# Optimization experiments

Hardware: AMD Instinct MI355X
Metric: run time of the kernel (lower is better)

Reference implementation:

```python
import jax, jax.numpy as jnp
import numpy as np

DIM = 1024
DEPTH = 7
PAR = 8
N_NODES = 2 ** (DEPTH + 1) - 1  # 255
WIDTH = PAR * N_NODES  # 2040


def setup_inputs() -> dict:
    key = jax.random.key(0)
    k1, k2, k3, k4 = jax.random.split(key, 4)
    init_k = float(np.sqrt(1.0 / DIM))
    init_k2 = float(np.sqrt(1.0 / ((DEPTH + 1) * PAR)))
    oldx = jax.random.normal(k1, (4, 2048, DIM), dtype=jnp.float32)
    W_in = jax.random.uniform(k2, (WIDTH, DIM), jnp.float32, -init_k, init_k)
    b_in = jax.random.uniform(k3, (WIDTH,), jnp.float32, -init_k, init_k)
    W_out = jax.random.uniform(k4, (DIM, WIDTH), jnp.float32, -init_k2, init_k2)
    return {"oldx": oldx, "W_in": W_in, "b_in": b_in, "W_out": W_out}


def reference(oldx, W_in, b_in, W_out):
    x = oldx.reshape(-1, DIM)                      # [B, dim]
    B = x.shape[0]
    logits = x @ W_in.T + b_in                     # [B, width] dense GEMM over ALL nodes
    decisions = (logits > 0).astype(jnp.int32).reshape(B, PAR, N_NODES)
    acts = jax.nn.silu(logits).reshape(B, PAR, N_NODES)

    # Tree traversal: mark root, then descend DEPTH levels by each node's sign bit.
    current = jnp.zeros((B, PAR), dtype=jnp.int32)
    dmap = jax.nn.one_hot(current, N_NODES, dtype=acts.dtype)  # root node marked
    for d in range(DEPTH):
        cur_platform = 2 ** d - 1
        next_platform = 2 ** (d + 1) - 1
        moves = jnp.take_along_axis(decisions, current[..., None], axis=2)[..., 0]
        current = (current - cur_platform) * 2 + moves + next_platform
        dmap = dmap + jax.nn.one_hot(current, N_NODES, dtype=acts.dtype)

    masked = acts * jax.lax.stop_gradient(dmap)    # only depth+1 nodes per tree survive
    out = masked.reshape(B, WIDTH) @ W_out.T       # [B, dim]
    return out.reshape(oldx.shape)
```

## Files before the change

kernel.cpp:

```cpp
#include <hip/hip_runtime.h>
#include <math.h>

#define DIM 1024
#define DEPTH 7
#define PAR 8
#define N_NODES 255
#define WIDTH 2040
#define MARGIN 0.01f

#define REPLANE(p) ((((p) & 1) << 3) | ((((p) >> 1) & 1) << 4) | ((((p) >> 2) & 1) << 5))

typedef _Float16 half2v __attribute__((ext_vector_type(2)));

__device__ __forceinline__ half2v as_h2(unsigned int u) {
    union { unsigned int u; half2v h; } c; c.u = u; return c.h;
}
__device__ __forceinline__ unsigned int pack_h2(float a, float b) {
    union { half2v h; unsigned int u; } c;
    c.h = (half2v){(_Float16)a, (_Float16)b};
    return c.u;
}

__device__ __forceinline__ float dot2h(unsigned int a, unsigned int b, float c) {
#if __has_builtin(__builtin_amdgcn_fdot2)
    return __builtin_amdgcn_fdot2(as_h2(a), as_h2(b), c, false);
#else
    half2v ha = as_h2(a), hb = as_h2(b);
    c = fmaf((float)ha.x, (float)hb.x, c);
    return fmaf((float)ha.y, (float)hb.y, c);
#endif
}

__device__ __forceinline__ float foldK(float a, float b, int K) {
    const bool hi = (threadIdx.x & (unsigned)K) != 0;
    const float keep = hi ? b : a;
    const float send = hi ? a : b;
    return keep + __shfl_xor(send, K, 64);
}

#define TRANS_BLOCKS 512

__global__ __launch_bounds__(256) void prep_kernel(
    const float* __restrict__ W_out,
    const float* __restrict__ W_in,
    unsigned short* __restrict__ WoT,
    unsigned int* __restrict__ Wh)
{
    __shared__ float tile[64][65];
    if (blockIdx.x < TRANS_BLOCKS) {
        const int w0 = (int)(blockIdx.x & 31) * 64;
        const int d0 = (int)(blockIdx.x >> 5) * 64;
        const int tid = (int)threadIdx.x;
        const int sub = tid & 15;
        const int grp = tid >> 4;

        #pragma unroll
        for (int pass = 0; pass < 4; ++pass) {
            const int dl = pass * 16 + grp;
            const int wl = sub * 4;
            const int w = w0 + wl;
            const int d = d0 + dl;
            float4 v = make_float4(0.f, 0.f, 0.f, 0.f);
            if (w + 3 < WIDTH) {
                v = *(const float4*)(W_out + (size_t)d * WIDTH + w);
            } else {
                float t0 = (w + 0 < WIDTH) ? W_out[(size_t)d * WIDTH + w + 0] : 0.f;
                float t1 = (w + 1 < WIDTH) ? W_out[(size_t)d * WIDTH + w + 1] : 0.f;
                float t2 = (w + 2 < WIDTH) ? W_out[(size_t)d * WIDTH + w + 2] : 0.f;
                float t3 = (w + 3 < WIDTH) ? W_out[(size_t)d * WIDTH + w + 3] : 0.f;
                v = make_float4(t0, t1, t2, t3);
            }
            tile[dl][wl + 0] = v.x; tile[dl][wl + 1] = v.y;
            tile[dl][wl + 2] = v.z; tile[dl][wl + 3] = v.w;
        }
        __syncthreads();
        #pragma unroll
        for (int pass = 0; pass < 4; ++pass) {
            const int wl = pass * 16 + grp;
            const int dl = sub * 4;
            const int w = w0 + wl;
            if (w < WIDTH) {
                uint2 pk;
                pk.x = pack_h2(tile[dl + 0][wl], tile[dl + 1][wl]);
                pk.y = pack_h2(tile[dl + 2][wl], tile[dl + 3][wl]);
                *(uint2*)(WoT + (size_t)w * DIM + d0 + dl) = pk;
            }
        }
    } else {
        const int n4 = WIDTH * DIM / 4;
        const int nthr = ((int)gridDim.x - TRANS_BLOCKS) * 256;
        for (int i = ((int)blockIdx.x - TRANS_BLOCKS) * 256 + (int)threadIdx.x;
             i < n4; i += nthr) {
            float4 v = ((const float4*)W_in)[i];
            uint2 pk;
            pk.x = pack_h2(v.x, v.y);
            pk.y = pack_h2(v.z, v.w);
            ((uint2*)Wh)[i] = pk;
        }
    }
}

__global__ __launch_bounds__(256) void fff_stage1_kernel(
    const float* __restrict__ x,
    const float* __restrict__ W_in,
    const float* __restrict__ b_in,
    const unsigned int* __restrict__ Wh,
    float* __restrict__ acts,
    unsigned short* __restrict__ gidx_out,
    int B)
{
    const int wv = (int)((blockIdx.x * blockDim.x + threadIdx.x) >> 6);
    const int lane = (int)(threadIdx.x & 63);
    const int rowA = wv * 2;
    const int rowB = wv * 2 + 1;
    if (rowA >= B) return;
    const bool hasB = (rowB < B);

    const float* xrA = x + (size_t)rowA * DIM;
    const float* xrB = x + (size_t)(hasB ? rowB : rowA) * DIM;

    unsigned int xpA[8], xpB[8];
    {
        float4 a0 = *(const float4*)(xrA + lane * 8 + 0);
        float4 a1 = *(const float4*)(xrA + lane * 8 + 4);
        float4 a2 = *(const float4*)(xrA + 512 + lane * 8 + 0);
        float4 a3 = *(const float4*)(xrA + 512 + lane * 8 + 4);
        xpA[0] = pack_h2(a0.x, a0.y); xpA[1] = pack_h2(a0.z, a0.w);
        xpA[2] = pack_h2(a1.x, a1.y); xpA[3] = pack_h2(a1.z, a1.w);
        xpA[4] = pack_h2(a2.x, a2.y); xpA[5] = pack_h2(a2.z, a2.w);
        xpA[6] = pack_h2(a3.x, a3.y); xpA[7] = pack_h2(a3.z, a3.w);
        float4 b0 = *(const float4*)(xrB + lane * 8 + 0);
        float4 b1 = *(const float4*)(xrB + lane * 8 + 4);
        float4 b2 = *(const float4*)(xrB + 512 + lane * 8 + 0);
        float4 b3 = *(const float4*)(xrB + 512 + lane * 8 + 4);
        xpB[0] = pack_h2(b0.x, b0.y); xpB[1] = pack_h2(b0.z, b0.w);
        xpB[2] = pack_h2(b1.x, b1.y); xpB[3] = pack_h2(b1.z, b1.w);
        xpB[4] = pack_h2(b2.x, b2.y); xpB[5] = pack_h2(b2.z, b2.w);
        xpB[6] = pack_h2(b3.x, b3.y); xpB[7] = pack_h2(b3.z, b3.w);
    }

    unsigned long long nodesA = 0ULL, nodesB = 0ULL;
    const int myp = ((lane >> 3) & 1) | (((lane >> 4) & 1) << 1) | (((lane >> 5) & 1) << 2);

    #pragma unroll 1
    for (int d = 0; d <= DEPTH; ++d) {
        int gA[PAR], gB[PAR];
        #pragma unroll
        for (int p = 0; p < PAR; ++p) {
            gA[p] = p * N_NODES + (int)((nodesA >> (8 * p)) & 0xffULL);
            gB[p] = p * N_NODES + (int)((nodesB >> (8 * p)) & 0xffULL);
        }

        const int gaA = (lane & 8) ? gA[1] : gA[0];
        const int gbA = (lane & 8) ? gA[3] : gA[2];
        const int gcA = (lane & 8) ? gA[5] : gA[4];
        const int gdA = (lane & 8) ? gA[7] : gA[6];
        const int geA = (lane & 16) ? gbA : gaA;
        const int gfA = (lane & 16) ? gdA : gcA;
        const int gmineA = (lane & 32) ? gfA : geA;
        const float biasA = b_in[gmineA];
        const int gaB = (lane & 8) ? gB[1] : gB[0];
        const int gbB = (lane & 8) ? gB[3] : gB[2];
        const int gcB = (lane & 8) ? gB[5] : gB[4];
        const int gdB = (lane & 8) ? gB[7] : gB[6];
        const int geB = (lane & 16) ? gbB : gaB;
        const int gfB = (lane & 16) ? gdB : gcB;
        const int gmineB = (lane & 32) ? gfB : geB;
        const float biasB = b_in[gmineB];

        float pA[PAR], pB[PAR];
        uint4 a0, a1, b0, b1;
        {
            const unsigned int* wrA = Wh + (size_t)gA[0] * (DIM / 2);
            a0 = *(const uint4*)(wrA + lane * 4);
            a1 = *(const uint4*)(wrA + 256 + lane * 4);
            const unsigned int* wrB = Wh + (size_t)gB[0] * (DIM / 2);
            b0 = *(const uint4*)(wrB + lane * 4);
            b1 = *(const uint4*)(wrB + 256 + lane * 4);
        }
        #pragma unroll
        for (int p = 0; p < PAR; ++p) {
            uint4 na0 = a0, na1 = a1, nb0 = b0, nb1 = b1;
            if (p < PAR - 1) {
                const unsigned int* wrA = Wh + (size_t)gA[p + 1] * (DIM / 2);
                na0 = *(const uint4*)(wrA + lane * 4);
                na1 = *(const uint4*)(wrA + 256 + lane * 4);
                const unsigned int* wrB = Wh + (size_t)gB[p + 1] * (DIM / 2);
                nb0 = *(const uint4*)(wrB + lane * 4);
                nb1 = *(const uint4*)(wrB + 256 + lane * 4);
            }
            float s = 0.f;
            s = dot2h(xpA[0], a0.x, s);
            s = dot2h(xpA[1], a0.y, s);
            s = dot2h(xpA[2], a0.z, s);
            s = dot2h(xpA[3], a0.w, s);
            s = dot2h(xpA[4], a1.x, s);
            s = dot2h(xpA[5], a1.y, s);
            s = dot2h(xpA[6], a1.z, s);
            s = dot2h(xpA[7], a1.w, s);
            pA[p] = s;
            float t = 0.f;
            t = dot2h(xpB[0], b0.x, t);
            t = dot2h(xpB[1], b0.y, t);
            t = dot2h(xpB[2], b0.z, t);
            t = dot2h(xpB[3], b0.w, t);
            t = dot2h(xpB[4], b1.x, t);
            t = dot2h(xpB[5], b1.y, t);
            t = dot2h(xpB[6], b1.z, t);
            t = dot2h(xpB[7], b1.w, t);
            pB[p] = t;
            a0 = na0; a1 = na1; b0 = nb0; b1 = nb1;
        }

        const float cA01 = foldK(pA[0], pA[1], 8);
        const float cB01 = foldK(pB[0], pB[1], 8);
        const float cA23 = foldK(pA[2], pA[3], 8);
        const float cB23 = foldK(pB[2], pB[3], 8);
        const float cA45 = foldK(pA[4], pA[5], 8);
        const float cB45 = foldK(pB[4], pB[5], 8);
        const float cA67 = foldK(pA[6], pA[7], 8);
        const float cB67 = foldK(pB[6], pB[7], 8);
        const float dA0 = foldK(cA01, cA23, 16);
        const float dB0 = foldK(cB01, cB23, 16);
        const float dA1 = foldK(cA45, cA67, 16);
        const float dB1 = foldK(cB45, cB67, 16);
        float eA = foldK(dA0, dA1, 32);
        float eB = foldK(dB0, dB1, 32);
        eA += __shfl_xor(eA, 1, 64);  eB += __shfl_xor(eB, 1, 64);
        eA += __shfl_xor(eA, 2, 64);  eB += __shfl_xor(eB, 2, 64);
        eA += __shfl_xor(eA, 4, 64);  eB += __shfl_xor(eB, 4, 64);
        float myA = eA + biasA;
        float myB = eB + biasB;

        if (d < DEPTH) {
            const unsigned long long balA = __ballot(fabsf(myA) < MARGIN);
            unsigned rmA = 0;
            #pragma unroll
            for (int p = 0; p < PAR; ++p)
                rmA |= ((unsigned)((balA >> REPLANE(p)) & 1ULL)) << p;
            while (rmA) {
                const int p = __builtin_ctz(rmA); rmA &= (rmA - 1u);
                const int gi = p * N_NODES + (int)((nodesA >> (8 * p)) & 0xffULL);
                const float* wr = W_in + (size_t)gi * DIM;
                float s = 0.f;
                #pragma unroll
                for (int q = 0; q < 4; ++q) {
                    const int off = (q & 1) * 4 + (q >> 1) * 512 + lane * 8;
                    const float4 fx = *(const float4*)(xrA + off);
                    const float4 fw = *(const float4*)(wr + off);
                    s = fmaf(fx.x, fw.x, s); s = fmaf(fx.y, fw.y, s);
                    s = fmaf(fx.z, fw.z, s); s = fmaf(fx.w, fw.w, s);
                }
                #pragma unroll
                for (int off = 32; off >= 1; off >>= 1)
                    s += __shfl_xor(s, off, 64);
                const float lf = s + b_in[gi];
                myA = (myp == p) ? lf : myA;
            }
            const unsigned long long balB = __ballot(fabsf(myB) < MARGIN);
            unsigned rmB = 0;
            #pragma unroll
            for (int p = 0; p < PAR; ++p)
                rmB |= ((unsigned)((balB >> REPLANE(p)) & 1ULL)) << p;
            while (rmB) {
                const int p = __builtin_ctz(rmB); rmB &= (rmB - 1u);
                const int gi = p * N_NODES + (int)((nodesB >> (8 * p)) & 0xffULL);
                const float* wr = W_in + (size_t)gi * DIM;
                float s = 0.f;
                #pragma unroll
                for (int q = 0; q < 4; ++q) {
                    const int off = (q & 1) * 4 + (q >> 1) * 512 + lane * 8;
                    const float4 fx = *(const float4*)(xrB + off);
                    const float4 fw = *(const float4*)(wr + off);
                    s = fmaf(fx.x, fw.x, s); s = fmaf(fx.y, fw.y, s);
                    s = fmaf(fx.z, fw.z, s); s = fmaf(fx.w, fw.w, s);
                }
                #pragma unroll
                for (int off = 32; off >= 1; off >>= 1)
                    s += __shfl_xor(s, off, 64);
                const float lf = s + b_in[gi];
                myB = (myp == p) ? lf : myB;
            }
        }

        const float actA = myA / (1.0f + __expf(-myA));
        const float actB = myB / (1.0f + __expf(-myB));
        const unsigned long long posA = __ballot(myA > 0.0f);
        const unsigned long long posB = __ballot(myB > 0.0f);

        if ((lane & 7) == 0) {
            const int slotA = (rowA << 6) + (d << 3) + myp;
            acts[slotA] = actA;
            gidx_out[slotA] = (unsigned short)gmineA;
            if (hasB) {
                const int slotB = (rowB << 6) + (d << 3) + myp;
                acts[slotB] = actB;
                gidx_out[slotB] = (unsigned short)gmineB;
            }
        }

        if (d < DEPTH) {
            #pragma unroll
            for (int p = 0; p < PAR; ++p) {
                const int npA = (int)((nodesA >> (8 * p)) & 0xffULL);
                const unsigned long long nnA = (unsigned long long)
                    (2 * npA + 1 + (int)((posA >> REPLANE(p)) & 1ULL));
                nodesA = (nodesA & ~(0xffULL << (8 * p))) | (nnA << (8 * p));
                const int npB = (int)((nodesB >> (8 * p)) & 0xffULL);
                const unsigned long long nnB = (unsigned long long)
                    (2 * npB + 1 + (int)((posB >> REPLANE(p)) & 1ULL));
                nodesB = (nodesB & ~(0xffULL << (8 * p))) | (nnB << (8 * p));
            }
        }
    }
}

__global__ __launch_bounds__(256) void fff_stage2_kernel(
    const float* __restrict__ acts,
    const unsigned short* __restrict__ gidx16,
    const unsigned short* __restrict__ WoT,
    float* __restrict__ out,
    int B)
{
    const int wave = (int)((blockIdx.x * blockDim.x + threadIdx.x) >> 6);
    const int lane = (int)(threadIdx.x & 63);
    if (wave >= B) return;

    const int base = wave << 6;
    const float a_l = acts[base + lane];
    const int   g_l = (int)gidx16[base + lane];

    float acc[16];
    #pragma unroll
    for (int i = 0; i < 16; ++i) acc[i] = 0.f;

    #pragma unroll 4
    for (int e = 0; e < 64; ++e) {
        const float a_ = __shfl(a_l, e, 64);
        const int   g  = __shfl(g_l, e, 64);
        const unsigned short* wo = WoT + (size_t)g * DIM;
        const uint4 u0 = *(const uint4*)(wo + lane * 8);
        const uint4 u1 = *(const uint4*)(wo + 512 + lane * 8);
        half2v h_;
        h_ = as_h2(u0.x); acc[0]  = fmaf((float)h_.x, a_, acc[0]);  acc[1]  = fmaf((float)h_.y, a_, acc[1]);
        h_ = as_h2(u0.y); acc[2]  = fmaf((float)h_.x, a_, acc[2]);  acc[3]  = fmaf((float)h_.y, a_, acc[3]);
        h_ = as_h2(u0.z); acc[4]  = fmaf((float)h_.x, a_, acc[4]);  acc[5]  = fmaf((float)h_.y, a_, acc[5]);
        h_ = as_h2(u0.w); acc[6]  = fmaf((float)h_.x, a_, acc[6]);  acc[7]  = fmaf((float)h_.y, a_, acc[7]);
        h_ = as_h2(u1.x); acc[8]  = fmaf((float)h_.x, a_, acc[8]);  acc[9]  = fmaf((float)h_.y, a_, acc[9]);
        h_ = as_h2(u1.y); acc[10] = fmaf((float)h_.x, a_, acc[10]); acc[11] = fmaf((float)h_.y, a_, acc[11]);
        h_ = as_h2(u1.z); acc[12] = fmaf((float)h_.x, a_, acc[12]); acc[13] = fmaf((float)h_.y, a_, acc[13]);
        h_ = as_h2(u1.w); acc[14] = fmaf((float)h_.x, a_, acc[14]); acc[15] = fmaf((float)h_.y, a_, acc[15]);
    }

    float* orow = out + (size_t)wave * DIM;
    *(float4*)(orow + lane * 8 + 0)       = make_float4(acc[0],  acc[1],  acc[2],  acc[3]);
    *(float4*)(orow + lane * 8 + 4)       = make_float4(acc[4],  acc[5],  acc[6],  acc[7]);
    *(float4*)(orow + 512 + lane * 8 + 0) = make_float4(acc[8],  acc[9],  acc[10], acc[11]);
    *(float4*)(orow + 512 + lane * 8 + 4) = make_float4(acc[12], acc[13], acc[14], acc[15]);
}

__global__ __launch_bounds__(256) void fff_f16_kernel(
    const float* __restrict__ x,
    const float* __restrict__ W_in,
    const float* __restrict__ b_in,
    const unsigned int* __restrict__ Wh,
    const unsigned short* __restrict__ WoT,
    float* __restrict__ out,
    int B)
{
    const int wave = (int)((blockIdx.x * blockDim.x + threadIdx.x) >> 6);
    const int lane = (int)(threadIdx.x & 63);
    if (wave >= B) return;

    const float* xr = x + (size_t)wave * DIM;
    unsigned int xp[8];
    {
        float4 a0 = *(const float4*)(xr + lane * 8 + 0);
        float4 a1 = *(const float4*)(xr + lane * 8 + 4);
        float4 a2 = *(const float4*)(xr + 512 + lane * 8 + 0);
        float4 a3 = *(const float4*)(xr + 512 + lane * 8 + 4);
        xp[0] = pack_h2(a0.x, a0.y);
        xp[1] = pack_h2(a0.z, a0.w);
        xp[2] = pack_h2(a1.x, a1.y);
        xp[3] = pack_h2(a1.z, a1.w);
        xp[4] = pack_h2(a2.x, a2.y);
        xp[5] = pack_h2(a2.z, a2.w);
        xp[6] = pack_h2(a3.x, a3.y);
        xp[7] = pack_h2(a3.z, a3.w);
    }

    float acc[16];
    #pragma unroll
    for (int i = 0; i < 16; ++i) acc[i] = 0.f;

    unsigned long long nodes = 0ULL;
    const int myp = ((lane >> 3) & 1) | (((lane >> 4) & 1) << 1) | (((lane >> 5) & 1) << 2);

    #pragma unroll 1
    for (int d = 0; d <= DEPTH; ++d) {
        int gidx[PAR];
        #pragma unroll
        for (int p = 0; p < PAR; ++p) {
            const int np = (int)((nodes >> (8 * p)) & 0xffULL);
            gidx[p] = p * N_NODES + np;
        }

        const int ga = (lane & 8) ? gidx[1] : gidx[0];
        const int gb = (lane & 8) ? gidx[3] : gidx[2];
        const int gc = (lane & 8) ? gidx[5] : gidx[4];
        const int gd = (lane & 8) ? gidx[7] : gidx[6];
        const int ge = (lane & 16) ? gb : ga;
        const int gf = (lane & 16) ? gd : gc;
        const int gmine = (lane & 32) ? gf : ge;
        const float bias = b_in[gmine];

        float partial[PAR];
        #pragma unroll
        for (int p = 0; p < PAR; ++p) {
            const unsigned int* wr = Wh + (size_t)gidx[p] * (DIM / 2);
            const uint4 u0 = *(const uint4*)(wr + lane * 4);
            const uint4 u1 = *(const uint4*)(wr + 256 + lane * 4);
            float s = 0.f;
            s = dot2h(xp[0], u0.x, s);
            s = dot2h(xp[1], u0.y, s);
            s = dot2h(xp[2], u0.z, s);
            s = dot2h(xp[3], u0.w, s);
            s = dot2h(xp[4], u1.x, s);
            s = dot2h(xp[5], u1.y, s);
            s = dot2h(xp[6], u1.z, s);
            s = dot2h(xp[7], u1.w, s);
            partial[p] = s;
        }

        const float c01 = foldK(partial[0], partial[1], 8);
        const float c23 = foldK(partial[2], partial[3], 8);
        const float c45 = foldK(partial[4], partial[5], 8);
        const float c67 = foldK(partial[6], partial[7], 8);
        const float d0f = foldK(c01, c23, 16);
        const float d1f = foldK(c45, c67, 16);
        float e = foldK(d0f, d1f, 32);
        e += __shfl_xor(e, 1, 64);
        e += __shfl_xor(e, 2, 64);
        e += __shfl_xor(e, 4, 64);
        float my = e + bias;

        if (d < DEPTH) {
            const unsigned long long bal = __ballot(fabsf(my) < MARGIN);
            unsigned rm = 0;
            #pragma unroll
            for (int p = 0; p < PAR; ++p)
                rm |= ((unsigned)((bal >> REPLANE(p)) & 1ULL)) << p;
            if (rm) {
                while (rm) {
                    const int p = __builtin_ctz(rm); rm &= (rm - 1u);
                    const int np = (int)((nodes >> (8 * p)) & 0xffULL);
                    const int gi = p * N_NODES + np;
                    const float* wr = W_in + (size_t)gi * DIM;
                    float s = 0.f;
                    #pragma unroll
                    for (int q = 0; q < 4; ++q) {
                        const int off = (q & 1) * 4 + (q >> 1) * 512 + lane * 8;
                        const float4 fx = *(const float4*)(xr + off);
                        const float4 fw = *(const float4*)(wr + off);
                        s = fmaf(fx.x, fw.x, s); s = fmaf(fx.y, fw.y, s);
                        s = fmaf(fx.z, fw.z, s); s = fmaf(fx.w, fw.w, s);
                    }
                    #pragma unroll
                    for (int off = 32; off >= 1; off >>= 1)
                        s += __shfl_xor(s, off, 64);
                    const float lf = s + b_in[gi];
                    my = (myp == p) ? lf : my;
                }
            }
        }

        const float act_mine = my / (1.0f + __expf(-my));
        const unsigned long long pos = __ballot(my > 0.0f);

        float act[PAR];
        #pragma unroll
        for (int p = 0; p < PAR; ++p)
            act[p] = __shfl(act_mine, REPLANE(p), 64);

        #pragma unroll
        for (int p = 0; p < PAR; ++p) {
            const unsigned short* wo = WoT + (size_t)gidx[p] * DIM;
            const uint4 u0 = *(const uint4*)(wo + lane * 8);
            const uint4 u1 = *(const uint4*)(wo + 512 + lane * 8);
            const float a_ = act[p];
            half2v h_;
            h_ = as_h2(u0.x); acc[0]  = fmaf((float)h_.x, a_, acc[0]);  acc[1]  = fmaf((float)h_.y, a_, acc[1]);
            h_ = as_h2(u0.y); acc[2]  = fmaf((float)h_.x, a_, acc[2]);  acc[3]  = fmaf((float)h_.y, a_, acc[3]);
            h_ = as_h2(u0.z); acc[4]  = fmaf((float)h_.x, a_, acc[4]);  acc[5]  = fmaf((float)h_.y, a_, acc[5]);
            h_ = as_h2(u0.w); acc[6]  = fmaf((float)h_.x, a_, acc[6]);  acc[7]  = fmaf((float)h_.y, a_, acc[7]);
            h_ = as_h2(u1.x); acc[8]  = fmaf((float)h_.x, a_, acc[8]);  acc[9]  = fmaf((float)h_.y, a_, acc[9]);
            h_ = as_h2(u1.y); acc[10] = fmaf((float)h_.x, a_, acc[10]); acc[11] = fmaf((float)h_.y, a_, acc[11]);
            h_ = as_h2(u1.z); acc[12] = fmaf((float)h_.x, a_, acc[12]); acc[13] = fmaf((float)h_.y, a_, acc[13]);
            h_ = as_h2(u1.w); acc[14] = fmaf((float)h_.x, a_, acc[14]); acc[15] = fmaf((float)h_.y, a_, acc[15]);

            if (d < DEPTH) {
                const int np = (int)((nodes >> (8 * p)) & 0xffULL);
                const unsigned long long nn = (unsigned long long)
                    (2 * np + 1 + (int)((pos >> REPLANE(p)) & 1ULL));
                nodes = (nodes & ~(0xffULL << (8 * p))) | (nn << (8 * p));
            }
        }
    }

    float* orow = out + (size_t)wave * DIM;
    *(float4*)(orow + lane * 8 + 0)       = make_float4(acc[0],  acc[1],  acc[2],  acc[3]);
    *(float4*)(orow + lane * 8 + 4)       = make_float4(acc[4],  acc[5],  acc[6],  acc[7]);
    *(float4*)(orow + 512 + lane * 8 + 0) = make_float4(acc[8],  acc[9],  acc[10], acc[11]);
    *(float4*)(orow + 512 + lane * 8 + 4) = make_float4(acc[12], acc[13], acc[14], acc[15]);
}

__global__ __launch_bounds__(256) void fff_fallback_kernel(
    const float* __restrict__ x, const float* __restrict__ W_in,
    const float* __restrict__ b_in, const float* __restrict__ W_out,
    float* __restrict__ out, int B)
{
    const int wave = (int)((blockIdx.x * blockDim.x + threadIdx.x) >> 6);
    const int lane = (int)(threadIdx.x & 63);
    if (wave >= B) return;

    const float* xr = x + (size_t)wave * DIM;
    float4 x4[4];
    x4[0] = *(const float4*)(xr + lane * 8 + 0);
    x4[1] = *(const float4*)(xr + lane * 8 + 4);
    x4[2] = *(const float4*)(xr + 512 + lane * 8 + 0);
    x4[3] = *(const float4*)(xr + 512 + lane * 8 + 4);

    float acc[16];
    #pragma unroll
    for (int i = 0; i < 16; ++i) acc[i] = 0.f;
    int node[PAR];
    #pragma unroll
    for (int p = 0; p < PAR; ++p) node[p] = 0;

    for (int d = 0; d <= DEPTH; ++d) {
        #pragma unroll
        for (int p = 0; p < PAR; ++p) {
            const int gidx = p * N_NODES + node[p];
            const float* wr = W_in + (size_t)gidx * DIM;
            const float4 wa = *(const float4*)(wr + lane * 8 + 0);
            const float4 wb = *(const float4*)(wr + lane * 8 + 4);
            const float4 wc = *(const float4*)(wr + 512 + lane * 8 + 0);
            const float4 wd = *(const float4*)(wr + 512 + lane * 8 + 4);
            float s = 0.f;
            s = fmaf(x4[0].x, wa.x, s); s = fmaf(x4[0].y, wa.y, s);
            s = fmaf(x4[0].z, wa.z, s); s = fmaf(x4[0].w, wa.w, s);
            s = fmaf(x4[1].x, wb.x, s); s = fmaf(x4[1].y, wb.y, s);
            s = fmaf(x4[1].z, wb.z, s); s = fmaf(x4[1].w, wb.w, s);
            s = fmaf(x4[2].x, wc.x, s); s = fmaf(x4[2].y, wc.y, s);
            s = fmaf(x4[2].z, wc.z, s); s = fmaf(x4[2].w, wc.w, s);
            s = fmaf(x4[3].x, wd.x, s); s = fmaf(x4[3].y, wd.y, s);
            s = fmaf(x4[3].z, wd.z, s); s = fmaf(x4[3].w, wd.w, s);
            #pragma unroll
            for (int off = 32; off >= 1; off >>= 1)
                s += __shfl_xor(s, off, 64);
            const float logit = s + b_in[gidx];
            const float act = logit / (1.0f + __expf(-logit));
            #pragma unroll
            for (int k = 0; k < 2; ++k) {
                #pragma unroll
                for (int j = 0; j < 8; ++j) {
                    const int e = k * 512 + lane * 8 + j;
                    acc[k * 8 + j] = fmaf(act, W_out[(size_t)e * WIDTH + gidx], acc[k * 8 + j]);
                }
            }
            node[p] = 2 * node[p] + 1 + ((logit > 0.0f) ? 1 : 0);
        }
    }

    float* orow = out + (size_t)wave * DIM;
    *(float4*)(orow + lane * 8 + 0)       = make_float4(acc[0],  acc[1],  acc[2],  acc[3]);
    *(float4*)(orow + lane * 8 + 4)       = make_float4(acc[4],  acc[5],  acc[6],  acc[7]);
    *(float4*)(orow + 512 + lane * 8 + 0) = make_float4(acc[8],  acc[9],  acc[10], acc[11]);
    *(float4*)(orow + 512 + lane * 8 + 4) = make_float4(acc[12], acc[13], acc[14], acc[15]);
}

extern "C" void kernel_launch(void* const* d_in, const int* in_sizes, int n_in,
                              void* d_out, int out_size, void* d_ws, size_t ws_size,
                              hipStream_t stream) {
    const float* oldx  = (const float*)d_in[0];
    const float* W_in  = (const float*)d_in[1];
    const float* b_in  = (const float*)d_in[2];
    const float* W_out = (const float*)d_in[3];
    float* out = (float*)d_out;

    const int B = in_sizes[0] / DIM;

    const size_t half   = (size_t)WIDTH * DIM * sizeof(unsigned short);
    const size_t actsz  = (size_t)B * 64 * sizeof(float);
    const size_t idxsz  = (size_t)B * 64 * sizeof(unsigned short);
    const bool use_split = (d_ws != nullptr) && (ws_size >= 2 * half + actsz + idxsz);
    const bool use_lp    = (d_ws != nullptr) && (ws_size >= 2 * half);

    const int blocks = (B + 3) / 4;

    if (use_split) {
        unsigned short* WoT  = (unsigned short*)d_ws;
        unsigned int*   Wh   = (unsigned int*)((char*)d_ws + half);
        float*          acts = (float*)((char*)d_ws + 2 * half);
        unsigned short* gidx = (unsigned short*)((char*)d_ws + 2 * half + actsz);
        prep_kernel<<<TRANS_BLOCKS + 1024, 256, 0, stream>>>(W_out, W_in, WoT, Wh);
        const int wavesS1 = (B + 1) / 2;
        const int blocksS1 = (wavesS1 + 3) / 4;
        fff_stage1_kernel<<<blocksS1, 256, 0, stream>>>(oldx, W_in, b_in, Wh, acts, gidx, B);
        fff_stage2_kernel<<<blocks, 256, 0, stream>>>(acts, gidx, WoT, out, B);
    } else if (use_lp) {
        unsigned short* WoT = (unsigned short*)d_ws;
        unsigned int*   Wh  = (unsigned int*)((char*)d_ws + half);
        prep_kernel<<<TRANS_BLOCKS + 1024, 256, 0, stream>>>(W_out, W_in, WoT, Wh);
        fff_f16_kernel<<<blocks, 256, 0, stream>>>(oldx, W_in, b_in, Wh, WoT, out, B);
    } else {
        fff_fallback_kernel<<<blocks, 256, 0, stream>>>(oldx, W_in, b_in, W_out, out, B);
    }
}
```

Measured before the change: 179.1 us.

## Fuse tree-routing stage and output projection into one two-row-per-wave kernel

Merges the two-stage split (a stage-1 kernel writing activations and node indices to workspace, then a stage-2 gather GEMV) into a single kernel. Each wave handles two rows, computes the routing logits, and immediately accumulates the selected W_out columns into register accumulators. This removes the intermediate workspace round-trip and one kernel launch. In exchange it doubles the accumulator registers (32 floats plus the packed x values), which may lower occupancy. It also removes the one-row-per-wave f16 kernel path.

```diff
diff --git a/kernel.cpp b/kernel.cpp
--- a/kernel.cpp
+++ b/kernel.cpp
@@ -100,13 +100,13 @@
     }
 }
 
-__global__ __launch_bounds__(256) void fff_stage1_kernel(
+__global__ __launch_bounds__(256) void fff_fused2_kernel(
     const float* __restrict__ x,
     const float* __restrict__ W_in,
     const float* __restrict__ b_in,
     const unsigned int* __restrict__ Wh,
-    float* __restrict__ acts,
-    unsigned short* __restrict__ gidx_out,
+    const unsigned short* __restrict__ WoT,
+    float* __restrict__ out,
     int B)
 {
     const int wv = (int)((blockIdx.x * blockDim.x + threadIdx.x) >> 6);
@@ -138,6 +138,10 @@
         xpB[4] = pack_h2(b2.x, b2.y); xpB[5] = pack_h2(b2.z, b2.w);
         xpB[6] = pack_h2(b3.x, b3.y); xpB[7] = pack_h2(b3.z, b3.w);
     }
+
+    float accA[16], accB[16];
+    #pragma unroll
+    for (int i = 0; i < 16; ++i) { accA[i] = 0.f; accB[i] = 0.f; }
 
     unsigned long long nodesA = 0ULL, nodesB = 0ULL;
     const int myp = ((lane >> 3) & 1) | (((lane >> 4) & 1) << 1) | (((lane >> 5) & 1) << 2);
@@ -288,15 +292,35 @@
         const unsigned long long posA = __ballot(myA > 0.0f);
         const unsigned long long posB = __ballot(myB > 0.0f);
 
-        if ((lane & 7) == 0) {
-            const int slotA = (rowA << 6) + (d << 3) + myp;
-            acts[slotA] = actA;
-            gidx_out[slotA] = (unsigned short)gmineA;
-            if (hasB) {
-                const int slotB = (rowB << 6) + (d << 3) + myp;
-                acts[slotB] = actB;
-                gidx_out[slotB] = (unsigned short)gmineB;
-            }
+        #pragma unroll
+        for (int p = 0; p < PAR; ++p) {
+            const int gAp = p * N_NODES + (int)((nodesA >> (8 * p)) & 0xffULL);
+            const float aA = __shfl(actA, REPLANE(p), 64);
+            const unsigned short* woA = WoT + (size_t)gAp * DIM;
+            const uint4 u0 = *(const uint4*)(woA + lane * 8);
+            const uint4 u1 = *(const uint4*)(woA + 512 + lane * 8);
+            const int gBp = p * N_NODES + (int)((nodesB >> (8 * p)) & 0xffULL);
+            const float aB = __shfl(actB, REPLANE(p), 64);
+            const unsigned short* woB = WoT + (size_t)gBp * DIM;
+            const uint4 v0 = *(const uint4*)(woB + lane * 8);
+            const uint4 v1 = *(const uint4*)(woB + 512 + lane * 8);
+            half2v h_;
+            h_ = as_h2(u0.x); accA[0]  = fmaf((float)h_.x, aA, accA[0]);  accA[1]  = fmaf((float)h_.y, aA, accA[1]);
+            h_ = as_h2(u0.y); accA[2]  = fmaf((float)h_.x, aA, accA[2]);  accA[3]  = fmaf((float)h_.y, aA, accA[3]);
+            h_ = as_h2(u0.z); accA[4]  = fmaf((float)h_.x, aA, accA[4]);  accA[5]  = fmaf((float)h_.y, aA, accA[5]);
+            h_ = as_h2(u0.w); accA[6]  = fmaf((float)h_.x, aA, accA[6]);  accA[7]  = fmaf((float)h_.y, aA, accA[7]);
+            h_ = as_h2(u1.x); accA[8]  = fmaf((float)h_.x, aA, accA[8]);  accA[9]  = fmaf((float)h_.y, aA, accA[9]);
+            h_ = as_h2(u1.y); accA[10] = fmaf((float)h_.x, aA, accA[10]); accA[11] = fmaf((float)h_.y, aA, accA[11]);
+            h_ = as_h2(u1.z); accA[12] = fmaf((float)h_.x, aA, accA[12]); accA[13] = fmaf((float)h_.y, aA, accA[13]);
+            h_ = as_h2(u1.w); accA[14] = fmaf((float)h_.x, aA, accA[14]); accA[15] = fmaf((float)h_.y, aA, accA[15]);
+            h_ = as_h2(v0.x); accB[0]  = fmaf((float)h_.x, aB, accB[0]);  accB[1]  = fmaf((float)h_.y, aB, accB[1]);
+            h_ = as_h2(v0.y); accB[2]  = fmaf((float)h_.x, aB, accB[2]);  accB[3]  = fmaf((float)h_.y, aB, accB[3]);
+            h_ = as_h2(v0.z); accB[4]  = fmaf((float)h_.x, aB, accB[4]);  accB[5]  = fmaf((float)h_.y, aB, accB[5]);
+            h_ = as_h2(v0.w); accB[6]  = fmaf((float)h_.x, aB, accB[6]);  accB[7]  = fmaf((float)h_.y, aB, accB[7]);
+            h_ = as_h2(v1.x); accB[8]  = fmaf((float)h_.x, aB, accB[8]);  accB[9]  = fmaf((float)h_.y, aB, accB[9]);
+            h_ = as_h2(v1.y); accB[10] = fmaf((float)h_.x, aB, accB[10]); accB[11] = fmaf((float)h_.y, aB, accB[11]);
+            h_ = as_h2(v1.z); accB[12] = fmaf((float)h_.x, aB, accB[12]); accB[13] = fmaf((float)h_.y, aB, accB[13]);
+            h_ = as_h2(v1.w); accB[14] = fmaf((float)h_.x, aB, accB[14]); accB[15] = fmaf((float)h_.y, aB, accB[15]);
         }
 
         if (d < DEPTH) {
@@ -313,205 +337,19 @@
             }
         }
     }
-}
-
-__global__ __launch_bounds__(256) void fff_stage2_kernel(
-    const float* __restrict__ acts,
-    const unsigned short* __restrict__ gidx16,
-    const unsigned short* __restrict__ WoT,
-    float* __restrict__ out,
-    int B)
-{
-    const int wave = (int)((blockIdx.x * blockDim.x + threadIdx.x) >> 6);
-    const int lane = (int)(threadIdx.x & 63);
-    if (wave >= B) return;
-
-    const int base = wave << 6;
-    const float a_l = acts[base + lane];
-    const int   g_l = (int)gidx16[base + lane];
-
-    float acc[16];
-    #pragma unroll
-    for (int i = 0; i < 16; ++i) acc[i] = 0.f;
-
-    #pragma unroll 4
-    for (int e = 0; e < 64; ++e) {
-        const float a_ = __shfl(a_l, e, 64);
-        const int   g  = __shfl(g_l, e, 64);
-        const unsigned short* wo = WoT + (size_t)g * DIM;
-        const uint4 u0 = *(const uint4*)(wo + lane * 8);
-        const uint4 u1 = *(const uint4*)(wo + 512 + lane * 8);
-        half2v h_;
-        h_ = as_h2(u0.x); acc[0]  = fmaf((float)h_.x, a_, acc[0]);  acc[1]  = fmaf((float)h_.y, a_, acc[1]);
-        h_ = as_h2(u0.y); acc[2]  = fmaf((float)h_.x, a_, acc[2]);  acc[3]  = fmaf((float)h_.y, a_, acc[3]);
-        h_ = as_h2(u0.z); acc[4]  = fmaf((float)h_.x, a_, acc[4]);  acc[5]  = fmaf((float)h_.y, a_, acc[5]);
-        h_ = as_h2(u0.w); acc[6]  = fmaf((float)h_.x, a_, acc[6]);  acc[7]  = fmaf((float)h_.y, a_, acc[7]);
-        h_ = as_h2(u1.x); acc[8]  = fmaf((float)h_.x, a_, acc[8]);  acc[9]  = fmaf((float)h_.y, a_, acc[9]);
-        h_ = as_h2(u1.y); acc[10] = fmaf((float)h_.x, a_, acc[10]); acc[11] = fmaf((float)h_.y, a_, acc[11]);
-        h_ = as_h2(u1.z); acc[12] = fmaf((float)h_.x, a_, acc[12]); acc[13] = fmaf((float)h_.y, a_, acc[13]);
-        h_ = as_h2(u1.w); acc[14] = fmaf((float)h_.x, a_, acc[14]); acc[15] = fmaf((float)h_.y, a_, acc[15]);
-    }
-
-    float* orow = out + (size_t)wave * DIM;
-    *(float4*)(orow + lane * 8 + 0)       = make_float4(acc[0],  acc[1],  acc[2],  acc[3]);
-    *(float4*)(orow + lane * 8 + 4)       = make_float4(acc[4],  acc[5],  acc[6],  acc[7]);
-    *(float4*)(orow + 512 + lane * 8 + 0) = make_float4(acc[8],  acc[9],  acc[10], acc[11]);
-    *(float4*)(orow + 512 + lane * 8 + 4) = make_float4(acc[12], acc[13], acc[14], acc[15]);
-}
-
-__global__ __launch_bounds__(256) void fff_f16_kernel(
-    const float* __restrict__ x,
-    const float* __restrict__ W_in,
-    const float* __restrict__ b_in,
-    const unsigned int* __restrict__ Wh,
-    const unsigned short* __restrict__ WoT,
-    float* __restrict__ out,
-    int B)
-{
-    const int wave = (int)((blockIdx.x * blockDim.x + threadIdx.x) >> 6);
-    const int lane = (int)(threadIdx.x & 63);
-    if (wave >= B) return;
-
-    const float* xr = x + (size_t)wave * DIM;
-    unsigned int xp[8];
-    {
-        float4 a0 = *(const float4*)(xr + lane * 8 + 0);
-        float4 a1 = *(const float4*)(xr + lane * 8 + 4);
-        float4 a2 = *(const float4*)(xr + 512 + lane * 8 + 0);
-        float4 a3 = *(const float4*)(xr + 512 + lane * 8 + 4);
-        xp[0] = pack_h2(a0.x, a0.y);
-        xp[1] = pack_h2(a0.z, a0.w);
-        xp[2] = pack_h2(a1.x, a1.y);
-        xp[3] = pack_h2(a1.z, a1.w);
-        xp[4] = pack_h2(a2.x, a2.y);
-        xp[5] = pack_h2(a2.z, a2.w);
-        xp[6] = pack_h2(a3.x, a3.y);
-        xp[7] = pack_h2(a3.z, a3.w);
-    }
-
-    float acc[16];
-    #pragma unroll
-    for (int i = 0; i < 16; ++i) acc[i] = 0.f;
-
-    unsigned long long nodes = 0ULL;
-    const int myp = ((lane >> 3) & 1) | (((lane >> 4) & 1) << 1) | (((lane >> 5) & 1) << 2);
-
-    #pragma unroll 1
-    for (int d = 0; d <= DEPTH; ++d) {
-        int gidx[PAR];
-        #pragma unroll
-        for (int p = 0; p < PAR; ++p) {
-            const int np = (int)((nodes >> (8 * p)) & 0xffULL);
-            gidx[p] = p * N_NODES + np;
-        }
-
-        const int ga = (lane & 8) ? gidx[1] : gidx[0];
-        const int gb = (lane & 8) ? gidx[3] : gidx[2];
-        const int gc = (lane & 8) ? gidx[5] : gidx[4];
-        const int gd = (lane & 8) ? gidx[7] : gidx[6];
-        const int ge = (lane & 16) ? gb : ga;
-        const int gf = (lane & 16) ? gd : gc;
-        const int gmine = (lane & 32) ? gf : ge;
-        const float bias = b_in[gmine];
-
-        float partial[PAR];
-        #pragma unroll
-        for (int p = 0; p < PAR; ++p) {
-            const unsigned int* wr = Wh + (size_t)gidx[p] * (DIM / 2);
-            const uint4 u0 = *(const uint4*)(wr + lane * 4);
-            const uint4 u1 = *(const uint4*)(wr + 256 + lane * 4);
-            float s = 0.f;
-            s = dot2h(xp[0], u0.x, s);
-            s = dot2h(xp[1], u0.y, s);
-            s = dot2h(xp[2], u0.z, s);
-            s = dot2h(xp[3], u0.w, s);
-            s = dot2h(xp[4], u1.x, s);
-            s = dot2h(xp[5], u1.y, s);
-            s = dot2h(xp[6], u1.z, s);
-            s = dot2h(xp[7], u1.w, s);
-            partial[p] = s;
-        }
-
-        const float c01 = foldK(partial[0], partial[1], 8);
-        const float c23 = foldK(partial[2], partial[3], 8);
-        const float c45 = foldK(partial[4], partial[5], 8);
-        const float c67 = foldK(partial[6], partial[7], 8);
-        const float d0f = foldK(c01, c23, 16);
-        const float d1f = foldK(c45, c67, 16);
-        float e = foldK(d0f, d1f, 32);
-        e += __shfl_xor(e, 1, 64);
-        e += __shfl_xor(e, 2, 64);
-        e += __shfl_xor(e, 4, 64);
-        float my = e + bias;
-
-        if (d < DEPTH) {
-            const unsigned long long bal = __ballot(fabsf(my) < MARGIN);
-            unsigned rm = 0;
-            #pragma unroll
-            for (int p = 0; p < PAR; ++p)
-                rm |= ((unsigned)((bal >> REPLANE(p)) & 1ULL)) << p;
-            if (rm) {
-                while (rm) {
-                    const int p = __builtin_ctz(rm); rm &= (rm - 1u);
-                    const int np = (int)((nodes >> (8 * p)) & 0xffULL);
-                    const int gi = p * N_NODES + np;
-                    const float* wr = W_in + (size_t)gi * DIM;
-                    float s = 0.f;
-                    #pragma unroll
-                    for (int q = 0; q < 4; ++q) {
-                        const int off = (q & 1) * 4 + (q >> 1) * 512 + lane * 8;
-                        const float4 fx = *(const float4*)(xr + off);
-                        const float4 fw = *(const float4*)(wr + off);
-                        s = fmaf(fx.x, fw.x, s); s = fmaf(fx.y, fw.y, s);
-                        s = fmaf(fx.z, fw.z, s); s = fmaf(fx.w, fw.w, s);
-                    }
-                    #pragma unroll
-                    for (int off = 32; off >= 1; off >>= 1)
-                        s += __shfl_xor(s, off, 64);
-                    const float lf = s + b_in[gi];
-                    my = (myp == p) ? lf : my;
-                }
-            }
-        }
-
-        const float act_mine = my / (1.0f + __expf(-my));
-        const unsigned long long pos = __ballot(my > 0.0f);
-
-        float act[PAR];
-        #pragma unroll
-        for (int p = 0; p < PAR; ++p)
-            act[p] = __shfl(act_mine, REPLANE(p), 64);
-
-        #pragma unroll
-        for (int p = 0; p < PAR; ++p) {
-            const unsigned short* wo = WoT + (size_t)gidx[p] * DIM;
-            const uint4 u0 = *(const uint4*)(wo + lane * 8);
-            const uint4 u1 = *(const uint4*)(wo + 512 + lane * 8);
-            const float a_ = act[p];
-            half2v h_;
-            h_ = as_h2(u0.x); acc[0]  = fmaf((float)h_.x, a_, acc[0]);  acc[1]  = fmaf((float)h_.y, a_, acc[1]);
-            h_ = as_h2(u0.y); acc[2]  = fmaf((float)h_.x, a_, acc[2]);  acc[3]  = fmaf((float)h_.y, a_, acc[3]);
-            h_ = as_h2(u0.z); acc[4]  = fmaf((float)h_.x, a_, acc[4]);  acc[5]  = fmaf((float)h_.y, a_, acc[5]);
-            h_ = as_h2(u0.w); acc[6]  = fmaf((float)h_.x, a_, acc[6]);  acc[7]  = fmaf((float)h_.y, a_, acc[7]);
-            h_ = as_h2(u1.x); acc[8]  = fmaf((float)h_.x, a_, acc[8]);  acc[9]  = fmaf((float)h_.y, a_, acc[9]);
-            h_ = as_h2(u1.y); acc[10] = fmaf((float)h_.x, a_, acc[10]); acc[11] = fmaf((float)h_.y, a_, acc[11]);
-            h_ = as_h2(u1.z); acc[12] = fmaf((float)h_.x, a_, acc[12]); acc[13] = fmaf((float)h_.y, a_, acc[13]);
-            h_ = as_h2(u1.w); acc[14] = fmaf((float)h_.x, a_, acc[14]); acc[15] = fmaf((float)h_.y, a_, acc[15]);
-
-            if (d < DEPTH) {
-                const int np = (int)((nodes >> (8 * p)) & 0xffULL);
-                const unsigned long long nn = (unsigned long long)
-                    (2 * np + 1 + (int)((pos >> REPLANE(p)) & 1ULL));
-                nodes = (nodes & ~(0xffULL << (8 * p))) | (nn << (8 * p));
-            }
-        }
-    }
-
-    float* orow = out + (size_t)wave * DIM;
-    *(float4*)(orow + lane * 8 + 0)       = make_float4(acc[0],  acc[1],  acc[2],  acc[3]);
-    *(float4*)(orow + lane * 8 + 4)       = make_float4(acc[4],  acc[5],  acc[6],  acc[7]);
-    *(float4*)(orow + 512 + lane * 8 + 0) = make_float4(acc[8],  acc[9],  acc[10], acc[11]);
-    *(float4*)(orow + 512 + lane * 8 + 4) = make_float4(acc[12], acc[13], acc[14], acc[15]);
+
+    float* orowA = out + (size_t)rowA * DIM;
+    *(float4*)(orowA + lane * 8 + 0)       = make_float4(accA[0],  accA[1],  accA[2],  accA[3]);
+    *(float4*)(orowA + lane * 8 + 4)       = make_float4(accA[4],  accA[5],  accA[6],  accA[7]);
+    *(float4*)(orowA + 512 + lane * 8 + 0) = make_float4(accA[8],  accA[9],  accA[10], accA[11]);
+    *(float4*)(orowA + 512 + lane * 8 + 4) = make_float4(accA[12], accA[13], accA[14], accA[15]);
+    if (hasB) {
+        float* orowB = out + (size_t)rowB * DIM;
+        *(float4*)(orowB + lane * 8 + 0)       = make_float4(accB[0],  accB[1],  accB[2],  accB[3]);
+        *(float4*)(orowB + lane * 8 + 4)       = make_float4(accB[4],  accB[5],  accB[6],  accB[7]);
+        *(float4*)(orowB + 512 + lane * 8 + 0) = make_float4(accB[8],  accB[9],  accB[10], accB[11]);
+        *(float4*)(orowB + 512 + lane * 8 + 4) = make_float4(accB[12], accB[13], accB[14], accB[15]);
+    }
 }
 
 __global__ __launch_bounds__(256) void fff_fallback_kernel(
@@ -590,30 +428,18 @@
 
     const int B = in_sizes[0] / DIM;
 
-    const size_t half   = (size_t)WIDTH * DIM * sizeof(unsigned short);
-    const size_t actsz  = (size_t)B * 64 * sizeof(float);
-    const size_t idxsz  = (size_t)B * 64 * sizeof(unsigned short);
-    const bool use_split = (d_ws != nullptr) && (ws_size >= 2 * half + actsz + idxsz);
-    const bool use_lp    = (d_ws != nullptr) && (ws_size >= 2 * half);
-
-    const int blocks = (B + 3) / 4;
-
-    if (use_split) {
-        unsigned short* WoT  = (unsigned short*)d_ws;
-        unsigned int*   Wh   = (unsigned int*)((char*)d_ws + half);
-        float*          acts = (float*)((char*)d_ws + 2 * half);
-        unsigned short* gidx = (unsigned short*)((char*)d_ws + 2 * half + actsz);
-        prep_kernel<<<TRANS_BLOCKS + 1024, 256, 0, stream>>>(W_out, W_in, WoT, Wh);
-        const int wavesS1 = (B + 1) / 2;
-        const int blocksS1 = (wavesS1 + 3) / 4;
-        fff_stage1_kernel<<<blocksS1, 256, 0, stream>>>(oldx, W_in, b_in, Wh, acts, gidx, B);
-        fff_stage2_kernel<<<blocks, 256, 0, stream>>>(acts, gidx, WoT, out, B);
-    } else if (use_lp) {
+    const size_t half = (size_t)WIDTH * DIM * sizeof(unsigned short);
+    const bool use_lp = (d_ws != nullptr) && (ws_size >= 2 * half);
+
+    if (use_lp) {
         unsigned short* WoT = (unsigned short*)d_ws;
         unsigned int*   Wh  = (unsigned int*)((char*)d_ws + half);
         prep_kernel<<<TRANS_BLOCKS + 1024, 256, 0, stream>>>(W_out, W_in, WoT, Wh);
-        fff_f16_kernel<<<blocks, 256, 0, stream>>>(oldx, W_in, b_in, Wh, WoT, out, B);
+        const int waves = (B + 1) / 2;
+        const int blocks = (waves + 3) / 4;
+        fff_fused2_kernel<<<blocks, 256, 0, stream>>>(oldx, W_in, b_in, Wh, WoT, out, B);
     } else {
+        const int blocks = (B + 3) / 4;
         fff_fallback_kernel<<<blocks, 256, 0, stream>>>(oldx, W_in, b_in, W_out, out, B);
     }
 }
```

Measured after the change: 176.3 us. Within noise of the previous version (-1.6%).
